# Optimization experiments

Hardware: AMD Instinct MI355X
Metric: run time of the kernel (lower is better)

## Reference

```python
import jax, jax.numpy as jnp
import numpy as np

WS = 7    # window_size
SS = 3    # shift_size
NH = 12   # num_heads


def _rel_index(ws):
    # doublestepseq(2*Ww-1, Wh, 1, Ww): seq1[:,None]+seq2[None,:] -> (1, N)
    seq1 = np.arange(ws) * (2 * ws - 1)
    coords = (seq1[:, None] + np.arange(ws)[None, :]).reshape(1, -1)  # (1, N)
    rel = coords + coords.T          # (N, N)
    return np.ascontiguousarray(rel[:, ::-1])  # flip along axis 1


def _attn_mask(Hp, Wp, ws, ss):
    img = np.zeros((Hp, Wp), np.int32)
    cnt = 0
    for h in (slice(0, -ws), slice(-ws, -ss), slice(-ss, None)):
        for w in (slice(0, -ws), slice(-ws, -ss), slice(-ss, None)):
            img[h, w] = cnt
            cnt += 1
    mw = img.reshape(Hp // ws, ws, Wp // ws, ws).transpose(0, 2, 1, 3).reshape(-1, ws * ws)
    diff = mw[:, None, :] - mw[:, :, None]  # unsqueeze(1) - unsqueeze(2)
    return np.where(diff != 0, -100.0, 0.0).astype(np.float32)  # (nW, N, N)


def setup_inputs() -> dict:
    key = jax.random.key(0)
    ks = jax.random.split(key, 4)
    B, H, W, C = 8, 112, 112, 384
    x = jax.random.normal(ks[0], (B, H * W, C), jnp.float32)
    qkv_w = jax.random.normal(ks[1], (C, 3 * C), jnp.float32) * 0.02
    qkv_b = jnp.zeros((3 * C,), jnp.float32)
    proj_w = jax.random.normal(ks[2], (C, C), jnp.float32) * 0.02
    proj_b = jnp.zeros((C,), jnp.float32)
    rel_pos_table = jax.random.normal(ks[3], ((2 * WS - 1) ** 2, NH), jnp.float32) * 0.02
    return {"x": x, "qkv_w": qkv_w, "qkv_b": qkv_b, "proj_w": proj_w,
            "proj_b": proj_b, "rel_pos_table": rel_pos_table, "H": H, "W": W}


def reference(x, qkv_w, qkv_b, proj_w, proj_b, rel_pos_table, H, W):
    B, L, C = x.shape
    hd = C // NH
    scale = hd ** -0.5
    N = WS * WS
    q = x.reshape(B, H, W, C)
    pad_r = (WS - W % WS) % WS
    pad_b = (WS - H % WS) % WS
    q = jnp.pad(q, ((0, 0), (0, pad_b), (0, pad_r), (0, 0)))
    Hp, Wp = H + pad_b, W + pad_r
    # cyclic shift
    sq = jnp.roll(q, (-SS, -SS), axis=(1, 2))
    nWh, nWw = Hp // WS, Wp // WS
    nW = nWh * nWw
    # window partition -> (B*nW, N, C)
    win = sq.reshape(B, nWh, WS, nWw, WS, C).transpose(0, 1, 3, 2, 4, 5).reshape(-1, N, C)
    Bw = win.shape[0]
    qkv = (win @ qkv_w + qkv_b).reshape(Bw, N, 3, NH, hd).transpose(2, 0, 3, 1, 4)
    qh, kh, vh = qkv[0], qkv[1], qkv[2]          # (Bw, NH, N, hd)
    attn = jnp.einsum('whnd,whmd->whnm', qh * scale, kh)  # (Bw, NH, N, N)
    # relative position bias
    ridx = _rel_index(WS)
    bias = rel_pos_table[ridx.reshape(-1)].reshape(N, N, NH).transpose(2, 0, 1)
    attn = attn + bias[None]
    # shifted-window mask
    mask = jnp.asarray(_attn_mask(Hp, Wp, WS, SS))  # (nW, N, N)
    attn = attn.reshape(B, nW, NH, N, N) + mask[None, :, None]
    attn = jax.nn.softmax(attn.reshape(Bw, NH, N, N), axis=-1)
    out = jnp.einsum('whnm,whmd->whnd', attn, vh).transpose(0, 2, 1, 3).reshape(Bw, N, C)
    out = out @ proj_w + proj_b
    # window reverse + reverse shift
    sx = out.reshape(B, nWh, nWw, WS, WS, C).transpose(0, 1, 3, 2, 4, 5).reshape(B, Hp, Wp, C)
    xr = jnp.roll(sx, (SS, SS), axis=(1, 2))[:, :H, :W, :]
    return xr.reshape(B, H * W, C)
```

## Files before the change

kernel.cpp:

```cpp
#include <hip/hip_runtime.h>


typedef __bf16 bf16;
typedef __bf16 bf16x8 __attribute__((ext_vector_type(8)));
typedef float  f32x4  __attribute__((ext_vector_type(4)));

#define MFMA16(a, b, c) __builtin_amdgcn_mfma_f32_16x16x32_bf16((a), (b), (c), 0, 0, 0)

static __device__ __forceinline__ bf16x8 cvt8(const float4 lo, const float4 hi) {
    bf16x8 r;
    r[0] = (bf16)lo.x; r[1] = (bf16)lo.y; r[2] = (bf16)lo.z; r[3] = (bf16)lo.w;
    r[4] = (bf16)hi.x; r[5] = (bf16)hi.y; r[6] = (bf16)hi.z; r[7] = (bf16)hi.w;
    return r;
}

__global__ __launch_bounds__(256) void k0_prep(
    const float* __restrict__ qkv_w, const float* __restrict__ proj_w,
    const float* __restrict__ rpt,
    bf16* __restrict__ w1t, bf16* __restrict__ w2t, float* __restrict__ BT)
{
    unsigned tid = blockIdx.x * 256u + threadIdx.x;
    if (tid < 442368u) {
        unsigned n = tid / 384u, k = tid - n * 384u;
        float v = qkv_w[k * 1152u + n];
        if (n < 384u) v *= 0.17677669529663687f;
        w1t[tid] = (bf16)v;
    } else if (tid < 589824u) {
        unsigned i = tid - 442368u;
        unsigned n = i / 384u, k = i - n * 384u;
        w2t[i] = (bf16)proj_w[k * 384u + n];
    } else if (tid < 638976u) {
        unsigned i = tid - 589824u;
        unsigned h = i >> 12, r = i & 4095u, b = r >> 6, a = r & 63u;
        float v;
        if (b >= 49u) v = -1e9f;
        else if (a >= 49u) v = 0.0f;
        else {
            int ia = (int)(a / 7u), ja = (int)(a - 7u * (a / 7u));
            int ib = (int)(b / 7u), jb = (int)(b - 7u * (b / 7u));
            int ridx = 84 + 13 * (ia - ib) + (ja - jb);
            v = rpt[ridx * 12 + (int)h];
        }
        BT[i] = v;
    }
}

__global__ __launch_bounds__(256, 3) void k1_qkv(
    const float* __restrict__ X, const bf16* __restrict__ W,
    const float* __restrict__ bias, bf16* __restrict__ Y)
{
    __shared__ __align__(16) bf16 Bs[24576];
    unsigned id = blockIdx.x;
    unsigned xcd = id & 7u, seq = id >> 3;
    unsigned mi = seq / 18u, nb = seq - mi * 18u;
    unsigned mblk = xcd + (mi << 3);
    unsigned tid = threadIdx.x;
    unsigned lane = tid & 63u, wv = tid >> 6;
    unsigned ln = lane & 15u, lq = lane >> 4;
    unsigned m0 = mblk * 256u, n0 = nb * 64u;

    for (unsigned c = tid; c < 3072u; c += 256u) {
        unsigned row = c / 48u, kc = c - row * 48u, k = kc * 8u;
        unsigned blk = (k >> 5) * 4u + (row >> 4);
        unsigned l = (row & 15u) | ((kc & 3u) << 4);
        *(int4*)&Bs[(blk * 64u + l) * 8u] = *(const int4*)(W + (size_t)(n0 + row) * 384u + k);
    }
    __syncthreads();

    f32x4 acc[4][4] = {};
    unsigned rbase = m0 + wv * 64u;

#pragma unroll
    for (unsigned kt = 0; kt < 12; ++kt) {
        bf16x8 af[4], bfr[4];
#pragma unroll
        for (unsigned i = 0; i < 4; ++i) {
            const float* p = X + (size_t)(rbase + i * 16u + ln) * 384u + kt * 32u + lq * 8u;
            af[i] = cvt8(*(const float4*)p, *(const float4*)(p + 4));
        }
#pragma unroll
        for (unsigned j = 0; j < 4; ++j)
            bfr[j] = *(const bf16x8*)&Bs[((kt * 4u + j) * 64u + lane) * 8u];
#pragma unroll
        for (unsigned i = 0; i < 4; ++i)
#pragma unroll
            for (unsigned j = 0; j < 4; ++j)
                acc[i][j] = MFMA16(af[i], bfr[j], acc[i][j]);
    }

#pragma unroll
    for (unsigned j = 0; j < 4; ++j) {
        unsigned col = n0 + j * 16u + ln;
        float bv = bias[col];
        if (col < 384u) bv *= 0.17677669529663687f;
#pragma unroll
        for (unsigned i = 0; i < 4; ++i) {
            unsigned row = rbase + i * 16u + lq * 4u;
#pragma unroll
            for (unsigned rg = 0; rg < 4; ++rg)
                Y[(size_t)(row + rg) * 1152u + col] = (bf16)(acc[i][j][rg] + bv);
        }
    }
}

__global__ __launch_bounds__(64) void k2_attn(
    bf16* __restrict__ Y, const float* __restrict__ BT)
{
    __shared__ __align__(16) bf16 Pl[64 * 72];
    __shared__ __align__(16) bf16 Vt[32 * 72];
    unsigned h = blockIdx.x, bwin = blockIdx.y;
    unsigned bb = bwin >> 8, wi = bwin & 255u, wh = wi >> 4, ww = wi & 15u;
    unsigned lane = threadIdx.x, ln = lane & 15u, lq = lane >> 4;
    unsigned hw32 = h * 32u;

    auto pixrow = [&](unsigned t) -> unsigned {
        unsigned ti = t / 7u, tj = t - ti * 7u;
        unsigned gh = wh * 7u + ti + 3u; if (gh >= 112u) gh -= 112u;
        unsigned gw = ww * 7u + tj + 3u; if (gw >= 112u) gw -= 112u;
        return bb * 12544u + gh * 112u + gw;
    };

    {
        unsigned t = lane < 49u ? lane : 0u;
        const bf16* vs = Y + (size_t)pixrow(t) * 1152u + 768u + hw32;
        bf16x8 v0 = *(const bf16x8*)(vs);
        bf16x8 v1 = *(const bf16x8*)(vs + 8);
        bf16x8 v2 = *(const bf16x8*)(vs + 16);
        bf16x8 v3 = *(const bf16x8*)(vs + 24);
#pragma unroll
        for (int d = 0; d < 8; ++d) {
            Vt[(unsigned)(d     ) * 72u + lane] = v0[d];
            Vt[(unsigned)(d + 8 ) * 72u + lane] = v1[d];
            Vt[(unsigned)(d + 16) * 72u + lane] = v2[d];
            Vt[(unsigned)(d + 24) * 72u + lane] = v3[d];
        }
    }

    bf16x8 qf[4], kf[4];
#pragma unroll
    for (int i = 0; i < 4; ++i) {
        unsigned t = (unsigned)i * 16u + ln; t = t < 49u ? t : 0u;
        qf[i] = *(const bf16x8*)(Y + (size_t)pixrow(t) * 1152u + hw32 + lq * 8u);
    }
#pragma unroll
    for (int i = 0; i < 4; ++i) {
        unsigned t = (unsigned)i * 16u + ln; t = t < 49u ? t : 0u;
        kf[i] = *(const bf16x8*)(Y + (size_t)pixrow(t) * 1152u + 384u + hw32 + lq * 8u);
    }

    f32x4 s[4][4] = {};
#pragma unroll
    for (int i = 0; i < 4; ++i)
#pragma unroll
        for (int j = 0; j < 4; ++j)
            s[i][j] = MFMA16(qf[i], kf[j], s[i][j]);

    const float* bth = BT + h * 4096u;
#pragma unroll
    for (int i = 0; i < 4; ++i)
#pragma unroll
        for (int j = 0; j < 4; ++j) {
            f32x4 b = *(const f32x4*)(bth + ((unsigned)j * 16u + ln) * 64u +
                                      (unsigned)i * 16u + lq * 4u);
            s[i][j] += b;
        }

    if (wh == 15u || ww == 15u) {
        int ra[4][4], rb[4];
#pragma unroll
        for (int i = 0; i < 4; ++i)
#pragma unroll
            for (int rg = 0; rg < 4; ++rg) {
                unsigned a = (unsigned)i * 16u + lq * 4u + (unsigned)rg;
                unsigned ti = a / 7u, tj = a - ti * 7u;
                unsigned gh = wh * 7u + ti, gw = ww * 7u + tj;
                int rh = gh < 105u ? 0 : (gh < 109u ? 1 : 2);
                int rw = gw < 105u ? 0 : (gw < 109u ? 1 : 2);
                ra[i][rg] = rh * 3 + rw;
            }
#pragma unroll
        for (int j = 0; j < 4; ++j) {
            unsigned bc = (unsigned)j * 16u + ln;
            unsigned ti = bc / 7u, tj = bc - ti * 7u;
            unsigned gh = wh * 7u + ti, gw = ww * 7u + tj;
            int rh = gh < 105u ? 0 : (gh < 109u ? 1 : 2);
            int rw = gw < 105u ? 0 : (gw < 109u ? 1 : 2);
            rb[j] = rh * 3 + rw;
        }
#pragma unroll
        for (int i = 0; i < 4; ++i)
#pragma unroll
            for (int j = 0; j < 4; ++j)
#pragma unroll
                for (int rg = 0; rg < 4; ++rg)
                    if (ra[i][rg] != rb[j]) s[i][j][rg] -= 100.0f;
    }

    float rinv[4][4];
#pragma unroll
    for (int i = 0; i < 4; ++i)
#pragma unroll
        for (int rg = 0; rg < 4; ++rg) {
            float m = fmaxf(fmaxf(s[i][0][rg], s[i][1][rg]),
                            fmaxf(s[i][2][rg], s[i][3][rg]));
#pragma unroll
            for (int d = 8; d >= 1; d >>= 1) m = fmaxf(m, __shfl_xor(m, d, 64));
            float sum = 0.0f;
#pragma unroll
            for (int j = 0; j < 4; ++j) {
                float e = __expf(s[i][j][rg] - m);
                s[i][j][rg] = e;
                sum += e;
            }
#pragma unroll
            for (int d = 8; d >= 1; d >>= 1) sum += __shfl_xor(sum, d, 64);
            rinv[i][rg] = 1.0f / sum;
        }

#pragma unroll
    for (int i = 0; i < 4; ++i)
#pragma unroll
        for (int rg = 0; rg < 4; ++rg) {
            unsigned a = (unsigned)i * 16u + lq * 4u + (unsigned)rg;
#pragma unroll
            for (int j = 0; j < 4; ++j)
                Pl[a * 72u + (unsigned)j * 16u + ln] = (bf16)s[i][j][rg];
        }

    __syncthreads();

    f32x4 o[4][2] = {};
#pragma unroll
    for (int ks = 0; ks < 2; ++ks) {
        bf16x8 pf[4], vf[2];
#pragma unroll
        for (int i = 0; i < 4; ++i)
            pf[i] = *(const bf16x8*)&Pl[((unsigned)i * 16u + ln) * 72u +
                                        (unsigned)ks * 32u + lq * 8u];
#pragma unroll
        for (int c = 0; c < 2; ++c)
            vf[c] = *(const bf16x8*)&Vt[((unsigned)c * 16u + ln) * 72u +
                                        (unsigned)ks * 32u + lq * 8u];
#pragma unroll
        for (int i = 0; i < 4; ++i)
#pragma unroll
            for (int c = 0; c < 2; ++c)
                o[i][c] = MFMA16(pf[i], vf[c], o[i][c]);
    }

#pragma unroll
    for (int i = 0; i < 4; ++i)
#pragma unroll
        for (int rg = 0; rg < 4; ++rg) {
            unsigned a = (unsigned)i * 16u + lq * 4u + (unsigned)rg;
            if (a < 49u) {
                float ri = rinv[i][rg];
                size_t base = (size_t)pixrow(a) * 1152u + hw32;
                Y[base + ln]       = (bf16)(o[i][0][rg] * ri);
                Y[base + 16u + ln] = (bf16)(o[i][1][rg] * ri);
            }
        }
}

__global__ __launch_bounds__(256, 3) void k3_proj(
    const bf16* __restrict__ A, const bf16* __restrict__ W,
    const float* __restrict__ bias, float* __restrict__ Out)
{
    __shared__ __align__(16) bf16 Bs[24576];
    unsigned id = blockIdx.x;
    unsigned xcd = id & 7u, seq = id >> 3;
    unsigned mi = seq / 6u, nb = seq - mi * 6u;
    unsigned mblk = xcd + (mi << 3);
    unsigned tid = threadIdx.x;
    unsigned lane = tid & 63u, wv = tid >> 6;
    unsigned ln = lane & 15u, lq = lane >> 4;
    unsigned m0 = mblk * 256u, n0 = nb * 64u;

    for (unsigned c = tid; c < 3072u; c += 256u) {
        unsigned row = c / 48u, kc = c - row * 48u, k = kc * 8u;
        unsigned blk = (k >> 5) * 4u + (row >> 4);
        unsigned l = (row & 15u) | ((kc & 3u) << 4);
        *(int4*)&Bs[(blk * 64u + l) * 8u] = *(const int4*)(W + (size_t)(n0 + row) * 384u + k);
    }
    __syncthreads();

    f32x4 acc[4][4] = {};
    unsigned rbase = m0 + wv * 64u;

#pragma unroll
    for (unsigned kt = 0; kt < 12; ++kt) {
        bf16x8 af[4], bfr[4];
#pragma unroll
        for (unsigned i = 0; i < 4; ++i)
            af[i] = *(const bf16x8*)(A + (size_t)(rbase + i * 16u + ln) * 1152u +
                                     kt * 32u + lq * 8u);
#pragma unroll
        for (unsigned j = 0; j < 4; ++j)
            bfr[j] = *(const bf16x8*)&Bs[((kt * 4u + j) * 64u + lane) * 8u];
#pragma unroll
        for (unsigned i = 0; i < 4; ++i)
#pragma unroll
            for (unsigned j = 0; j < 4; ++j)
                acc[i][j] = MFMA16(af[i], bfr[j], acc[i][j]);
    }

#pragma unroll
    for (unsigned j = 0; j < 4; ++j) {
        unsigned col = n0 + j * 16u + ln;
        float bv = bias[col];
#pragma unroll
        for (unsigned i = 0; i < 4; ++i) {
            unsigned row = rbase + i * 16u + lq * 4u;
#pragma unroll
            for (unsigned rg = 0; rg < 4; ++rg)
                Out[(size_t)(row + rg) * 384u + col] = acc[i][j][rg] + bv;
        }
    }
}

extern "C" void kernel_launch(void* const* d_in, const int* in_sizes, int n_in,
                              void* d_out, int out_size, void* d_ws, size_t ws_size,
                              hipStream_t stream) {
    const float* x      = (const float*)d_in[0];
    const float* qkv_w  = (const float*)d_in[1];
    const float* qkv_b  = (const float*)d_in[2];
    const float* proj_w = (const float*)d_in[3];
    const float* proj_b = (const float*)d_in[4];
    const float* rpt    = (const float*)d_in[5];
    (void)in_sizes; (void)n_in; (void)out_size; (void)ws_size;

    char* ws = (char*)d_ws;
    bf16*  Y   = (bf16*)(ws);
    bf16*  w1t = (bf16*)(ws + 231211008u);
    bf16*  w2t = (bf16*)(ws + 232095744u);
    float* BT  = (float*)(ws + 232390656u);
    float* out = (float*)d_out;

    k0_prep<<<2496, 256, 0, stream>>>(qkv_w, proj_w, rpt, w1t, w2t, BT);
    k1_qkv<<<7056, 256, 0, stream>>>(x, w1t, qkv_b, Y);
    k2_attn<<<dim3(12, 2048), 64, 0, stream>>>(Y, BT);
    k3_proj<<<2352, 256, 0, stream>>>(Y, w2t, proj_b, out);
}
```

Measured before the change: 789.4 us.

## Pre-convert X to bf16 and pipeline A-fragment loads in QKV GEMM

Adds a separate kernel that converts the fp32 input to bf16 once, so the QKV GEMM reads half the bytes and skips repeated per-N-block conversion. The new GEMM prefetches A fragments two k-steps ahead using a triple-buffered register array, and stages the output tile through shared memory for coalesced stores. The cost is an extra full read and write pass over the input, extra workspace, and more registers. The new path only runs when the workspace is large enough, otherwise the old kernel is kept.

```diff
diff --git a/kernel.cpp b/kernel.cpp
--- a/kernel.cpp
+++ b/kernel.cpp
@@ -45,8 +45,17 @@
     }
 }
 
-__global__ __launch_bounds__(256, 3) void k1_qkv(
-    const float* __restrict__ X, const bf16* __restrict__ W,
+__global__ __launch_bounds__(256) void k0x_cvt(
+    const float* __restrict__ X, bf16* __restrict__ Xb)
+{
+    size_t base = ((size_t)blockIdx.x * 256u + threadIdx.x) * 8u;
+    float4 lo = *(const float4*)(X + base);
+    float4 hi = *(const float4*)(X + base + 4);
+    *(bf16x8*)(Xb + base) = cvt8(lo, hi);
+}
+
+__global__ __launch_bounds__(256, 3) void k1_qkv_b(
+    const bf16* __restrict__ X, const bf16* __restrict__ W,
     const float* __restrict__ bias, bf16* __restrict__ Y)
 {
     __shared__ __align__(16) bf16 Bs[24576];
@@ -69,6 +78,86 @@
 
     f32x4 acc[4][4] = {};
     unsigned rbase = m0 + wv * 64u;
+    const bf16* Ab = X + (size_t)(rbase + ln) * 384u + lq * 8u;
+
+    bf16x8 af[3][4];
+#pragma unroll
+    for (unsigned i = 0; i < 4; ++i) af[0][i] = *(const bf16x8*)(Ab + i * 6144u);
+#pragma unroll
+    for (unsigned i = 0; i < 4; ++i) af[1][i] = *(const bf16x8*)(Ab + 32u + i * 6144u);
+
+#pragma unroll
+    for (unsigned kt = 0; kt < 12; ++kt) {
+        if (kt < 10u) {
+#pragma unroll
+            for (unsigned i = 0; i < 4; ++i)
+                af[(kt + 2u) % 3u][i] =
+                    *(const bf16x8*)(Ab + (kt + 2u) * 32u + i * 6144u);
+        }
+        bf16x8 bfr[4];
+#pragma unroll
+        for (unsigned j = 0; j < 4; ++j)
+            bfr[j] = *(const bf16x8*)&Bs[((kt * 4u + j) * 64u + lane) * 8u];
+#pragma unroll
+        for (unsigned i = 0; i < 4; ++i)
+#pragma unroll
+            for (unsigned j = 0; j < 4; ++j)
+                acc[i][j] = MFMA16(af[kt % 3u][i], bfr[j], acc[i][j]);
+    }
+
+    float bv[4];
+#pragma unroll
+    for (unsigned j = 0; j < 4; ++j) {
+        unsigned col = n0 + j * 16u + ln;
+        bv[j] = bias[col];
+        if (col < 384u) bv[j] *= 0.17677669529663687f;
+    }
+
+    __syncthreads();
+#pragma unroll
+    for (unsigned i = 0; i < 4; ++i)
+#pragma unroll
+        for (unsigned j = 0; j < 4; ++j)
+#pragma unroll
+            for (unsigned rg = 0; rg < 4; ++rg) {
+                unsigned r = wv * 64u + i * 16u + lq * 4u + rg;
+                Bs[r * 72u + j * 16u + ln] = (bf16)(acc[i][j][rg] + bv[j]);
+            }
+    __syncthreads();
+
+#pragma unroll
+    for (unsigned it = 0; it < 8; ++it) {
+        unsigned idx = it * 256u + tid;
+        unsigned row = idx >> 3, c8 = (idx & 7u) * 8u;
+        *(bf16x8*)(Y + (size_t)(m0 + row) * 1152u + n0 + c8) =
+            *(const bf16x8*)&Bs[row * 72u + c8];
+    }
+}
+
+__global__ __launch_bounds__(256, 3) void k1_qkv(
+    const float* __restrict__ X, const bf16* __restrict__ W,
+    const float* __restrict__ bias, bf16* __restrict__ Y)
+{
+    __shared__ __align__(16) bf16 Bs[24576];
+    unsigned id = blockIdx.x;
+    unsigned xcd = id & 7u, seq = id >> 3;
+    unsigned mi = seq / 18u, nb = seq - mi * 18u;
+    unsigned mblk = xcd + (mi << 3);
+    unsigned tid = threadIdx.x;
+    unsigned lane = tid & 63u, wv = tid >> 6;
+    unsigned ln = lane & 15u, lq = lane >> 4;
+    unsigned m0 = mblk * 256u, n0 = nb * 64u;
+
+    for (unsigned c = tid; c < 3072u; c += 256u) {
+        unsigned row = c / 48u, kc = c - row * 48u, k = kc * 8u;
+        unsigned blk = (k >> 5) * 4u + (row >> 4);
+        unsigned l = (row & 15u) | ((kc & 3u) << 4);
+        *(int4*)&Bs[(blk * 64u + l) * 8u] = *(const int4*)(W + (size_t)(n0 + row) * 384u + k);
+    }
+    __syncthreads();
+
+    f32x4 acc[4][4] = {};
+    unsigned rbase = m0 + wv * 64u;
 
 #pragma unroll
     for (unsigned kt = 0; kt < 12; ++kt) {
@@ -327,17 +416,23 @@
     const float* proj_w = (const float*)d_in[3];
     const float* proj_b = (const float*)d_in[4];
     const float* rpt    = (const float*)d_in[5];
-    (void)in_sizes; (void)n_in; (void)out_size; (void)ws_size;
+    (void)in_sizes; (void)n_in; (void)out_size;
 
     char* ws = (char*)d_ws;
     bf16*  Y   = (bf16*)(ws);
     bf16*  w1t = (bf16*)(ws + 231211008u);
     bf16*  w2t = (bf16*)(ws + 232095744u);
     float* BT  = (float*)(ws + 232390656u);
+    bf16*  Xb  = (bf16*)(ws + 232587264u);
     float* out = (float*)d_out;
 
     k0_prep<<<2496, 256, 0, stream>>>(qkv_w, proj_w, rpt, w1t, w2t, BT);
-    k1_qkv<<<7056, 256, 0, stream>>>(x, w1t, qkv_b, Y);
+    if (ws_size >= 309657600ull) {
+        k0x_cvt<<<18816, 256, 0, stream>>>(x, Xb);
+        k1_qkv_b<<<7056, 256, 0, stream>>>(Xb, w1t, qkv_b, Y);
+    } else {
+        k1_qkv<<<7056, 256, 0, stream>>>(x, w1t, qkv_b, Y);
+    }
     k2_attn<<<dim3(12, 2048), 64, 0, stream>>>(Y, BT);
     k3_proj<<<2352, 256, 0, stream>>>(Y, w2t, proj_b, out);
 }
```

New measurement: 679.3 us. 1.16x faster.
